# Performance work log

Measured on AMD Instinct MI355X. Metric: run time of the kernel, lower is better.

## Reference

```python
import jax, jax.numpy as jnp
import numpy as np

KH, KW = 3, 3
K = KH * KW
PAD, STRIDE, DIL = 1, 1, 1


def _conv(x, w, b):
    y = jax.lax.conv_general_dilated(
        x, w, (STRIDE, STRIDE), ((PAD, PAD), (PAD, PAD)),
        rhs_dilation=(DIL, DIL), dimension_numbers=('NCHW', 'OIHW', 'NCHW'))
    return y + b[None, :, None, None]


def _bilinear_gather(x, py, px):
    # x: [B,C,H,W]; py, px: float sample coords [B,K,Ho,Wo]. Zero outside bounds.
    B, C, H, W = x.shape
    y0 = jnp.floor(py)
    x0 = jnp.floor(px)
    wy1 = py - y0
    wx1 = px - x0
    wy0 = 1.0 - wy1
    wx0 = 1.0 - wx1
    xf = x.reshape(B, C, H * W)

    def g(yi, xi):
        valid = (yi >= 0) & (yi < H) & (xi >= 0) & (xi < W)
        yc = jnp.clip(yi, 0, H - 1).astype(jnp.int32)
        xc = jnp.clip(xi, 0, W - 1).astype(jnp.int32)
        idx = (yc * W + xc).reshape(B, -1)                      # [B, K*Ho*Wo]
        v = jax.vmap(lambda im, ix: im[:, ix])(xf, idx)         # [B, C, K*Ho*Wo]
        v = v.reshape(B, C, *yi.shape[1:])                      # [B,C,K,Ho,Wo]
        return v * valid[:, None].astype(x.dtype)

    return ((wy0 * wx0)[:, None] * g(y0, x0)
            + (wy0 * wx1)[:, None] * g(y0, x0 + 1)
            + (wy1 * wx0)[:, None] * g(y0 + 1, x0)
            + (wy1 * wx1)[:, None] * g(y0 + 1, x0 + 1))


def setup_inputs() -> dict:
    key = jax.random.key(0)
    k1, k2, k3 = jax.random.split(key, 3)
    B, C, H, W = 8, 256, 64, 64
    x = jax.random.normal(k1, (B, C, H, W), dtype=jnp.float32)
    # small init for offset/mask conv so predicted offsets stay modest (as in DCNv2 practice)
    w_om = jax.random.normal(k2, (3 * K, C, KH, KW), dtype=jnp.float32) * 0.01
    b_om = jnp.zeros((3 * K,), dtype=jnp.float32)
    w_dc = jax.random.normal(k3, (C, C, KH, KW), dtype=jnp.float32) * (1.0 / np.sqrt(C * K))
    b_dc = jnp.zeros((C,), dtype=jnp.float32)
    return {"x": x, "w_om": w_om, "b_om": b_om, "w_dc": w_dc, "b_dc": b_dc}


def reference(x, w_om, b_om, w_dc, b_dc):
    B, C, H, W = x.shape
    om = _conv(x, w_om, b_om)                      # [B, 3K, H, W]
    offset = om[:, :2 * K].reshape(B, K, 2, H, W)  # per-tap (dy, dx)
    mask = jax.nn.sigmoid(om[:, 2 * K:])           # [B, K, H, W]
    dy, dx = offset[:, :, 0], offset[:, :, 1]
    kh = jnp.repeat(jnp.arange(KH), KW)            # [K] kernel row index
    kw = jnp.tile(jnp.arange(KW), KH)              # [K] kernel col index
    ho = jnp.arange(H)
    wo = jnp.arange(W)
    py = ho[None, None, :, None] * STRIDE - PAD + kh[None, :, None, None] * DIL + dy
    px = wo[None, None, None, :] * STRIDE - PAD + kw[None, :, None, None] * DIL + dx
    sampled = _bilinear_gather(x, py, px)          # [B,C,K,H,W]
    sampled = sampled * mask[:, None]              # modulated (DCNv2)
    w = w_dc.reshape(w_dc.shape[0], C, K)
    out = jnp.einsum('bckhw,ock->bohw', sampled, w) + b_dc[None, :, None, None]
    return out
```

## Files before the change

### kernel.cpp

```cpp
#include <hip/hip_runtime.h>
#include <hip/hip_bf16.h>
#include <hip/hip_fp16.h>
#include <math.h>

#define BB   8
#define CIN  256
#define HH   64
#define WW   64
#define OMC  27
#define HW   (HH*WW)
#define KTOT (CIN*9)
#define NPIX 32
#define SPITCH 296
#define XP1    40
#define TPW    17

typedef short bf16x8 __attribute__((ext_vector_type(8)));
typedef float f32x4  __attribute__((ext_vector_type(4)));

__device__ __forceinline__ unsigned short f2bf(float f) {
    union { float f; unsigned int u; } v; v.f = f;
    unsigned int r = v.u + 0x7FFFu + ((v.u >> 16) & 1u);
    return (unsigned short)(r >> 16);
}
__device__ __forceinline__ float bflo(unsigned int a) {
    union { unsigned int u; float f; } c; c.u = a << 16; return c.f;
}
__device__ __forceinline__ float bfhi(unsigned int a) {
    union { unsigned int u; float f; } c; c.u = a & 0xFFFF0000u; return c.f;
}

__global__ __launch_bounds__(256) void wprep_kernel(
    const float* __restrict__ w_dc, unsigned short* __restrict__ wA)
{
    int e = blockIdx.x * 256 + threadIdx.x;
    int o = e / KTOT;
    int k = e - o * KTOT;
    int c   = k / 9;
    int tap = k - c * 9;
    int kp  = (c >> 5) * 288 + tap * 32 + (c & 31);
    wA[((size_t)(kp >> 3) * 256 + o) * 8 + (kp & 7)] = f2bf(w_dc[e]);
}

__global__ __launch_bounds__(256) void womprep_kernel(
    const float* __restrict__ w_om, unsigned short* __restrict__ wOmA)
{
    int e = blockIdx.x * 256 + threadIdx.x;
    int j  = e & 7;
    int t1 = e >> 3;
    int o  = t1 & 31;
    int t2 = t1 >> 5;
    int cb = t2 & 3;
    int t3 = t2 >> 2;
    int cc = t3 & 7;
    int tap = t3 >> 3;
    int c = cc * 32 + cb * 8 + j;
    float v = (o < OMC) ? w_om[(size_t)o * KTOT + c * 9 + tap] : 0.f;
    wOmA[e] = f2bf(v);
}

__global__ __launch_bounds__(512, 4) void deform_mfma_kernel(
    const float* __restrict__ x, const unsigned short* __restrict__ wOmA,
    const float* __restrict__ b_om,
    const unsigned short* __restrict__ wA, const float* __restrict__ b_dc,
    float* __restrict__ out)
{
    const int rawb = blockIdx.x;
    const int obid = ((rawb & 7) << 7) | (rawb >> 3);
    const int b    = obid >> 7;
    const int h    = (obid >> 1) & 63;
    const int w0   = (obid & 1) * NPIX;
    const int t    = threadIdx.x;
    const int wv   = t >> 6;
    const int lane = t & 63;
    const int lq   = lane >> 4;
    const int lm   = lane & 15;

    __shared__ __align__(16) unsigned short sS[NPIX * SPITCH];
    __shared__ __align__(16) unsigned short sR[8224];
    __shared__ __align__(16) int4 s_par[9 * NPIX];

    float* som  = reinterpret_cast<float*>(sS);
    unsigned short* bufA = sR;
    unsigned short* bufB = sR + 4080;

    const size_t xb_base = (size_t)b * CIN * HW;
    const float* gx_base = x + xb_base;

    int stg[7];
#pragma unroll
    for (int i = 0; i < 7; ++i) {
        int n = t + i * 512;
        if (n < 3200) {
            int slot = n / 200;
            int rc   = n - slot * 200;
            int r    = rc / 40;
            int c    = rc - r * 40;
            int gy   = min(max(h - 2 + r, 0), HH - 1);
            int gx   = min(max(w0 - 4 + c, 0), WW - 1);
            stg[i] = (rc * TPW + slot) | (slot << 12) | ((gy * WW + gx) << 16);
        } else stg[i] = -1;
    }

    {
        f32x4 accOm = (f32x4)(0.f);
        const int mfp = (wv >> 1) & 1;
        const int nfp = wv & 1;
        const int p   = nfp * 16 + lm;
        const bf16x8* wOmV = reinterpret_cast<const bf16x8*>(wOmA);

        auto stage1 = [&](int cc, unsigned short* dst) {
            const float* gch = gx_base + (size_t)cc * 32 * HW;
#pragma unroll
            for (int i = 0; i < 7; ++i) {
                int e = t + i * 512;
                if (e < 3264) {
                    int cl  = e / 102;
                    int rc  = e - cl * 102;
                    int row = rc / 34;
                    int col = rc - row * 34;
                    int gy  = h - 1 + row;
                    int gxx = w0 - 1 + col;
                    float v = 0.f;
                    if (gy >= 0 && gy < HH && (unsigned)gxx < WW)
                        v = gch[cl * HW + gy * WW + gxx];
                    dst[rc * XP1 + cl] = f2bf(v);
                }
            }
        };

        stage1(0, bufA);
        __syncthreads();
        for (int cc = 0; cc < 8; ++cc) {
            unsigned short* cur = (cc & 1) ? bufB : bufA;
            unsigned short* nxt = (cc & 1) ? bufA : bufB;
            if (cc < 7) stage1(cc + 1, nxt);
#pragma unroll
            for (int tap = 0; tap < 9; ++tap) {
                int kh = tap / 3, kw = tap % 3;
                bf16x8 bfr = *reinterpret_cast<const bf16x8*>(
                    &cur[(kh * 34 + p + kw) * XP1 + lq * 8]);
                bf16x8 af = wOmV[(((tap * 8 + cc) * 4 + lq) * 32) + mfp * 16 + lm];
                accOm = __builtin_amdgcn_mfma_f32_16x16x32_bf16(af, bfr, accOm, 0, 0, 0);
            }
            __syncthreads();
        }

        if (wv < 4) {
#pragma unroll
            for (int r = 0; r < 4; ++r) {
                int o = mfp * 16 + lq * 4 + r;
                if (o < OMC)
                    som[o * NPIX + p] = accOm[r] + b_om[o];
            }
        }
    }
    __syncthreads();

    float L0[7], L1[7];
    {
        const float* gch = gx_base;
#pragma unroll
        for (int i = 0; i < 7; ++i)
            if (stg[i] >= 0) {
                int sl = (stg[i] >> 12) & 0xF;
                int go = (stg[i] >> 16) & 0xFFF;
                L0[i] = gch[(size_t)(2 * sl) * HW + go];
                L1[i] = gch[(size_t)(2 * sl + 1) * HW + go];
            }
    }

    {
        unsigned int* tWw = reinterpret_cast<unsigned int*>(sR);
        for (int i = t; i < 712; i += 512) tWw[3400 + i] = 0u;
    }

    if (t < 9 * NPIX) {
        int tap = t >> 5;
        int pix = t & 31;
        float dy = som[(2 * tap) * NPIX + pix];
        float dx = som[(2 * tap + 1) * NPIX + pix];
        float mv = som[(18 + tap) * NPIX + pix];
        float m  = 1.f / (1.f + expf(-mv));
        float py = (float)(h - 1 + tap / 3) + dy;
        float px = (float)(w0 + pix - 1 + tap % 3) + dx;
        float y0f = floorf(py), x0f = floorf(px);
        float wy1 = py - y0f, wx1 = px - x0f;
        float wy0 = 1.f - wy1, wx0 = 1.f - wx1;
        int y0 = (int)y0f, x0 = (int)x0f;
        int y1 = y0 + 1, x1 = x0 + 1;
        bool yv0 = (y0 >= 0) && (y0 < HH);
        bool yv1 = (y1 >= 0) && (y1 < HH);
        bool xv0 = (x0 >= 0) && (x0 < WW);
        bool xv1 = (x1 >= 0) && (x1 < WW);
        int yc0 = min(max(y0, 0), HH - 1), yc1 = min(max(y1, 0), HH - 1);
        int xc0 = min(max(x0, 0), WW - 1), xc1 = min(max(x1, 0), WW - 1);
        float wwx = (yv0 && xv0) ? wy0 * wx0 * m : 0.f;
        float wwy = (yv0 && xv1) ? wy0 * wx1 * m : 0.f;
        float wwz = (yv1 && xv0) ? wy1 * wx0 * m : 0.f;
        float www = (yv1 && xv1) ? wy1 * wx1 * m : 0.f;
        if (xc1 == xc0) { wwx += wwy; wwy = 0.f; wwz += www; www = 0.f; }
        if (yc1 == yc0) { wwx += wwz; wwz = 0.f; wwy += www; www = 0.f; }
        bool inT = (yc0 >= h - 2) && (yc1 <= h + 2) &&
                   (xc0 >= w0 - 4) && (xc1 <= w0 + 35);
        int lb = (yc0 - (h - 2)) * 40 + (xc0 - (w0 - 4));
        int pk = (lb & 0xFF) | ((xc1 - xc0) << 8) | ((yc1 - yc0) << 9)
               | ((yc0 * WW + xc0) << 10);
        if (!inT) pk |= (int)0x80000000;
        __half2 wab = __floats2half2_rn(wwx, wwy);
        __half2 wcd = __floats2half2_rn(wwz, www);
        s_par[t] = make_int4(pk,
                             *reinterpret_cast<int*>(&wab),
                             *reinterpret_cast<int*>(&wcd), 0);
    }
    {
        unsigned int* tWw = reinterpret_cast<unsigned int*>(sR);
#pragma unroll
        for (int i = 0; i < 7; ++i)
            if (stg[i] >= 0)
                tWw[stg[i] & 0xFFF] =
                    f2bf(L0[i]) | ((unsigned int)f2bf(L1[i]) << 16);
    }
    __syncthreads();

    f32x4 acc[2][2];
#pragma unroll
    for (int i = 0; i < 2; ++i)
#pragma unroll
        for (int j = 0; j < 2; ++j)
            acc[i][j] = (f32x4)(0.f);

    const int pix  = t >> 4;
    const int slot = t & 15;
    const unsigned int* tW = reinterpret_cast<const unsigned int*>(sR);

    for (int ch = 0; ch < 8; ++ch) {
#pragma unroll 3
        for (int tap = 0; tap < 9; ++tap) {
            int idx = tap * NPIX + pix;
            int4 pv = s_par[idx];
            int pk  = pv.x;
            float2 wab = __half22float2(*reinterpret_cast<__half2*>(&pv.y));
            float2 wcd = __half22float2(*reinterpret_cast<__half2*>(&pv.z));
            float v0, v1;
            if (pk >= 0) {
                int base = (pk & 0xFF) * TPW + slot;
                unsigned int a00 = tW[base];
                unsigned int a01 = tW[base + TPW];
                unsigned int a10 = tW[base + 40 * TPW];
                unsigned int a11 = tW[base + 41 * TPW];
                v0 = wab.x * bflo(a00) + wab.y * bflo(a01)
                   + wcd.x * bflo(a10) + wcd.y * bflo(a11);
                v1 = wab.x * bfhi(a00) + wab.y * bfhi(a01)
                   + wcd.x * bfhi(a10) + wcd.y * bfhi(a11);
            } else {
                int off00 = (pk >> 10) & 0xFFF;
                int d01 = (pk >> 8) & 1;
                int d10 = ((pk >> 9) & 1) * WW;
                const float* xc = x + xb_base + (size_t)(ch * 32 + 2 * slot) * HW;
                v0 = wab.x * xc[off00]       + wab.y * xc[off00 + d01]
                   + wcd.x * xc[off00 + d10] + wcd.y * xc[off00 + d10 + d01];
                xc += HW;
                v1 = wab.x * xc[off00]       + wab.y * xc[off00 + d01]
                   + wcd.x * xc[off00 + d10] + wcd.y * xc[off00 + d10 + d01];
            }
            *reinterpret_cast<unsigned int*>(
                &sS[pix * SPITCH + tap * 32 + 2 * slot]) =
                f2bf(v0) | ((unsigned int)f2bf(v1) << 16);
        }
        __syncthreads();

        if (ch < 7) {
            const float* gch = gx_base + (size_t)(ch + 1) * 32 * HW;
#pragma unroll
            for (int i = 0; i < 7; ++i)
                if (stg[i] >= 0) {
                    int sl = (stg[i] >> 12) & 0xF;
                    int go = (stg[i] >> 16) & 0xFFF;
                    L0[i] = gch[(size_t)(2 * sl) * HW + go];
                    L1[i] = gch[(size_t)(2 * sl + 1) * HW + go];
                }
        }

        const int kb_base = ch * 36;
        const bf16x8* wAv = reinterpret_cast<const bf16x8*>(wA);
#pragma unroll 1
        for (int ks = 0; ks < 9; ++ks) {
            bf16x8 bfr[2];
#pragma unroll
            for (int nf = 0; nf < 2; ++nf)
                bfr[nf] = *reinterpret_cast<const bf16x8*>(
                    &sS[(nf * 16 + lm) * SPITCH + ks * 32 + lq * 8]);
#pragma unroll
            for (int mf = 0; mf < 2; ++mf) {
                int o  = wv * 32 + mf * 16 + lm;
                int kb = kb_base + ks * 4 + lq;
                bf16x8 af = wAv[(size_t)kb * 256 + o];
#pragma unroll
                for (int nf = 0; nf < 2; ++nf)
                    acc[mf][nf] = __builtin_amdgcn_mfma_f32_16x16x32_bf16(
                        af, bfr[nf], acc[mf][nf], 0, 0, 0);
            }
        }

        if (ch < 7) {
            unsigned int* tWw = reinterpret_cast<unsigned int*>(sR);
#pragma unroll
            for (int i = 0; i < 7; ++i)
                if (stg[i] >= 0)
                    tWw[stg[i] & 0xFFF] =
                        f2bf(L0[i]) | ((unsigned int)f2bf(L1[i]) << 16);
        }
        __syncthreads();
    }

#pragma unroll
    for (int mf = 0; mf < 2; ++mf) {
#pragma unroll
        for (int r = 0; r < 4; ++r) {
            int o = wv * 32 + mf * 16 + lq * 4 + r;
            float bo = b_dc[o];
#pragma unroll
            for (int nf = 0; nf < 2; ++nf) {
                int p = nf * 16 + lm;
                out[((size_t)(b * 256 + o)) * HW + h * WW + w0 + p] = acc[mf][nf][r] + bo;
            }
        }
    }
}

extern "C" void kernel_launch(void* const* d_in, const int* in_sizes, int n_in,
                              void* d_out, int out_size, void* d_ws, size_t ws_size,
                              hipStream_t stream) {
    const float* x    = (const float*)d_in[0];
    const float* w_om = (const float*)d_in[1];
    const float* b_om = (const float*)d_in[2];
    const float* w_dc = (const float*)d_in[3];
    const float* b_dc = (const float*)d_in[4];
    float* out = (float*)d_out;

    unsigned short* wA   = (unsigned short*)d_ws;
    unsigned short* wOmA = (unsigned short*)((char*)d_ws + 1179648);

    wprep_kernel<<<(256 * KTOT) / 256, 256, 0, stream>>>(w_dc, wA);
    womprep_kernel<<<73728 / 256, 256, 0, stream>>>(w_om, wOmA);
    deform_mfma_kernel<<<BB * HH * 2, 512, 0, stream>>>(x, wOmA, b_om, wA, b_dc, out);
}
```

Baseline: 152.3 us.

## Double-buffer staging and sample tiles to overlap gather with MFMA

Doubles both the bf16 input staging tile and the sampled-column tile in LDS. The bilinear gather for the next channel chunk, and the global load of the chunk after it, can then run in the same iteration as the MFMA GEMM on the current chunk. This removes one __syncthreads per chunk and is meant to hide gather and load latency behind matrix work. The cost is roughly double the LDS per block, which can lower the number of resident blocks per CU below the launch-bounds target of four.

```diff
diff --git a/kernel.cpp b/kernel.cpp
--- a/kernel.cpp
+++ b/kernel.cpp
@@ -12,8 +12,10 @@
 #define KTOT (CIN*9)
 #define NPIX 32
 #define SPITCH 296
+#define SSZ   (NPIX*SPITCH)
 #define XP1    40
 #define TPW    17
+#define TBUF   4096
 
 typedef short bf16x8 __attribute__((ext_vector_type(8)));
 typedef float f32x4  __attribute__((ext_vector_type(4)));
@@ -76,8 +78,8 @@
     const int lq   = lane >> 4;
     const int lm   = lane & 15;
 
-    __shared__ __align__(16) unsigned short sS[NPIX * SPITCH];
-    __shared__ __align__(16) unsigned short sR[8224];
+    __shared__ __align__(16) unsigned short sS[2 * SSZ];
+    __shared__ __align__(16) unsigned short sR[2 * TBUF * 2];
     __shared__ __align__(16) int4 s_par[9 * NPIX];
 
     float* som  = reinterpret_cast<float*>(sS);
@@ -157,9 +159,12 @@
     }
     __syncthreads();
 
+    unsigned int* tWw = reinterpret_cast<unsigned int*>(sR);
+    const unsigned int* tW = tWw;
+
     float L0[7], L1[7];
-    {
-        const float* gch = gx_base;
+    auto issueStage = [&](int ch) {
+        const float* gch = gx_base + (size_t)ch * 32 * HW;
 #pragma unroll
         for (int i = 0; i < 7; ++i)
             if (stg[i] >= 0) {
@@ -168,22 +173,73 @@
                 L0[i] = gch[(size_t)(2 * sl) * HW + go];
                 L1[i] = gch[(size_t)(2 * sl + 1) * HW + go];
             }
-    }
-
-    {
-        unsigned int* tWw = reinterpret_cast<unsigned int*>(sR);
-        for (int i = t; i < 712; i += 512) tWw[3400 + i] = 0u;
+    };
+    auto writeTile = [&](int buf) {
+        int off = buf << 12;
+#pragma unroll
+        for (int i = 0; i < 7; ++i)
+            if (stg[i] >= 0)
+                tWw[off + (stg[i] & 0xFFF)] =
+                    f2bf(L0[i]) | ((unsigned int)f2bf(L1[i]) << 16);
+    };
+
+    const int pix  = t >> 4;
+    const int slot = t & 15;
+
+    auto gather = [&](int ch) {
+        const int toff = (ch & 1) << 12;
+        unsigned short* sSc = sS + (ch & 1) * SSZ;
+#pragma unroll 3
+        for (int tap = 0; tap < 9; ++tap) {
+            int idx = tap * NPIX + pix;
+            int4 pv = s_par[idx];
+            int pk  = pv.x;
+            float2 wab = __half22float2(*reinterpret_cast<__half2*>(&pv.y));
+            float2 wcd = __half22float2(*reinterpret_cast<__half2*>(&pv.z));
+            float v0, v1;
+            if (pk >= 0) {
+                int base = toff + (pk & 0xFF) * TPW + slot;
+                unsigned int a00 = tW[base];
+                unsigned int a01 = tW[base + TPW];
+                unsigned int a10 = tW[base + 40 * TPW];
+                unsigned int a11 = tW[base + 41 * TPW];
+                v0 = wab.x * bflo(a00) + wab.y * bflo(a01)
+                   + wcd.x * bflo(a10) + wcd.y * bflo(a11);
+                v1 = wab.x * bfhi(a00) + wab.y * bfhi(a01)
+                   + wcd.x * bfhi(a10) + wcd.y * bfhi(a11);
+            } else {
+                int off00 = (pk >> 10) & 0xFFF;
+                int d01 = (pk >> 8) & 1;
+                int d10 = ((pk >> 9) & 1) * WW;
+                const float* xc = x + xb_base + (size_t)(ch * 32 + 2 * slot) * HW;
+                v0 = wab.x * xc[off00]       + wab.y * xc[off00 + d01]
+                   + wcd.x * xc[off00 + d10] + wcd.y * xc[off00 + d10 + d01];
+                xc += HW;
+                v1 = wab.x * xc[off00]       + wab.y * xc[off00 + d01]
+                   + wcd.x * xc[off00 + d10] + wcd.y * xc[off00 + d10 + d01];
+            }
+            *reinterpret_cast<unsigned int*>(
+                &sSc[pix * SPITCH + tap * 32 + 2 * slot]) =
+                f2bf(v0) | ((unsigned int)f2bf(v1) << 16);
+        }
+    };
+
+    issueStage(0);
+
+    for (int i = t; i < 1392; i += 512) {
+        int w = (i < 696) ? (3400 + i) : (4096 + 3400 + (i - 696));
+        tWw[w] = 0u;
     }
 
     if (t < 9 * NPIX) {
         int tap = t >> 5;
-        int pix = t & 31;
-        float dy = som[(2 * tap) * NPIX + pix];
-        float dx = som[(2 * tap + 1) * NPIX + pix];
-        float mv = som[(18 + tap) * NPIX + pix];
+        int pix2 = t & 31;
+        float dy = som[(2 * tap) * NPIX + pix2];
+        float dx = som[(2 * tap + 1) * NPIX + pix2];
+        float mv = som[(18 + tap) * NPIX + pix2];
         float m  = 1.f / (1.f + expf(-mv));
         float py = (float)(h - 1 + tap / 3) + dy;
-        float px = (float)(w0 + pix - 1 + tap % 3) + dx;
+        float px = (float)(w0 + pix2 - 1 + tap % 3) + dx;
         float y0f = floorf(py), x0f = floorf(px);
         float wy1 = py - y0f, wx1 = px - x0f;
         float wy0 = 1.f - wy1, wx0 = 1.f - wx1;
@@ -213,14 +269,12 @@
                              *reinterpret_cast<int*>(&wab),
                              *reinterpret_cast<int*>(&wcd), 0);
     }
-    {
-        unsigned int* tWw = reinterpret_cast<unsigned int*>(sR);
-#pragma unroll
-        for (int i = 0; i < 7; ++i)
-            if (stg[i] >= 0)
-                tWw[stg[i] & 0xFFF] =
-                    f2bf(L0[i]) | ((unsigned int)f2bf(L1[i]) << 16);
-    }
+    writeTile(0);
+    __syncthreads();
+
+    gather(0);
+    issueStage(1);
+    writeTile(1);
     __syncthreads();
 
     f32x4 acc[2][2];
@@ -230,67 +284,21 @@
         for (int j = 0; j < 2; ++j)
             acc[i][j] = (f32x4)(0.f);
 
-    const int pix  = t >> 4;
-    const int slot = t & 15;
-    const unsigned int* tW = reinterpret_cast<const unsigned int*>(sR);
+    const bf16x8* wAv = reinterpret_cast<const bf16x8*>(wA);
 
     for (int ch = 0; ch < 8; ++ch) {
-#pragma unroll 3
-        for (int tap = 0; tap < 9; ++tap) {
-            int idx = tap * NPIX + pix;
-            int4 pv = s_par[idx];
-            int pk  = pv.x;
-            float2 wab = __half22float2(*reinterpret_cast<__half2*>(&pv.y));
-            float2 wcd = __half22float2(*reinterpret_cast<__half2*>(&pv.z));
-            float v0, v1;
-            if (pk >= 0) {
-                int base = (pk & 0xFF) * TPW + slot;
-                unsigned int a00 = tW[base];
-                unsigned int a01 = tW[base + TPW];
-                unsigned int a10 = tW[base + 40 * TPW];
-                unsigned int a11 = tW[base + 41 * TPW];
-                v0 = wab.x * bflo(a00) + wab.y * bflo(a01)
-                   + wcd.x * bflo(a10) + wcd.y * bflo(a11);
-                v1 = wab.x * bfhi(a00) + wab.y * bfhi(a01)
-                   + wcd.x * bfhi(a10) + wcd.y * bfhi(a11);
-            } else {
-                int off00 = (pk >> 10) & 0xFFF;
-                int d01 = (pk >> 8) & 1;
-                int d10 = ((pk >> 9) & 1) * WW;
-                const float* xc = x + xb_base + (size_t)(ch * 32 + 2 * slot) * HW;
-                v0 = wab.x * xc[off00]       + wab.y * xc[off00 + d01]
-                   + wcd.x * xc[off00 + d10] + wcd.y * xc[off00 + d10 + d01];
-                xc += HW;
-                v1 = wab.x * xc[off00]       + wab.y * xc[off00 + d01]
-                   + wcd.x * xc[off00 + d10] + wcd.y * xc[off00 + d10 + d01];
-            }
-            *reinterpret_cast<unsigned int*>(
-                &sS[pix * SPITCH + tap * 32 + 2 * slot]) =
-                f2bf(v0) | ((unsigned int)f2bf(v1) << 16);
-        }
-        __syncthreads();
-
-        if (ch < 7) {
-            const float* gch = gx_base + (size_t)(ch + 1) * 32 * HW;
-#pragma unroll
-            for (int i = 0; i < 7; ++i)
-                if (stg[i] >= 0) {
-                    int sl = (stg[i] >> 12) & 0xF;
-                    int go = (stg[i] >> 16) & 0xFFF;
-                    L0[i] = gch[(size_t)(2 * sl) * HW + go];
-                    L1[i] = gch[(size_t)(2 * sl + 1) * HW + go];
-                }
-        }
-
+        if (ch < 6) issueStage(ch + 2);
+        if (ch < 7) gather(ch + 1);
+
+        const unsigned short* sSc = sS + (ch & 1) * SSZ;
         const int kb_base = ch * 36;
-        const bf16x8* wAv = reinterpret_cast<const bf16x8*>(wA);
 #pragma unroll 1
         for (int ks = 0; ks < 9; ++ks) {
             bf16x8 bfr[2];
 #pragma unroll
             for (int nf = 0; nf < 2; ++nf)
                 bfr[nf] = *reinterpret_cast<const bf16x8*>(
-                    &sS[(nf * 16 + lm) * SPITCH + ks * 32 + lq * 8]);
+                    &sSc[(nf * 16 + lm) * SPITCH + ks * 32 + lq * 8]);
 #pragma unroll
             for (int mf = 0; mf < 2; ++mf) {
                 int o  = wv * 32 + mf * 16 + lm;
@@ -303,14 +311,7 @@
             }
         }
 
-        if (ch < 7) {
-            unsigned int* tWw = reinterpret_cast<unsigned int*>(sR);
-#pragma unroll
-            for (int i = 0; i < 7; ++i)
-                if (stg[i] >= 0)
-                    tWw[stg[i] & 0xFFF] =
-                        f2bf(L0[i]) | ((unsigned int)f2bf(L1[i]) << 16);
-        }
+        if (ch < 6) writeTile(ch & 1);
         __syncthreads();
     }
 
```

Measured after the change: 156.0 us. 2.4% more time.

## Split offset/mask convolution into a separate full-row MFMA kernel

Applied to the files above, without the earlier changes.

Moves the offset/mask convolution out of the fused deformable kernel into its own kernel. Each block of the new kernel computes a full 64-pixel output row, using 2 M-fragments per wave, and writes the offsets and masks to a workspace buffer. The main kernel then reads the offsets from global memory instead of computing them, which removes the redundant halo staging and the 8-step synchronised prologue. The cost is an extra kernel launch plus a global round trip for the offset/mask tensor.

```diff
diff --git a/kernel.cpp b/kernel.cpp
--- a/kernel.cpp
+++ b/kernel.cpp
@@ -59,9 +59,83 @@
     wOmA[e] = f2bf(v);
 }
 
+__global__ __launch_bounds__(256, 4) void om_mfma_kernel(
+    const float* __restrict__ x, const unsigned short* __restrict__ wOmA,
+    const float* __restrict__ b_om, float* __restrict__ om)
+{
+    const int rawb = blockIdx.x;
+    const int obid = ((rawb & 7) << 6) | (rawb >> 3);
+    const int b    = obid >> 6;
+    const int h    = obid & 63;
+    const int t    = threadIdx.x;
+    const int wv   = t >> 6;
+    const int lane = t & 63;
+    const int lq   = lane >> 4;
+    const int lm   = lane & 15;
+    const int p    = wv * 16 + lm;
+
+    __shared__ __align__(16) unsigned short sX[2 * 3 * 66 * XP1];
+
+    unsigned short* bufA = sX;
+    unsigned short* bufB = sX + 3 * 66 * XP1;
+
+    const size_t xb_base = (size_t)b * CIN * HW;
+    const float* gx_base = x + xb_base;
+    const bf16x8* wOmV = reinterpret_cast<const bf16x8*>(wOmA);
+
+    f32x4 accOm[2];
+    accOm[0] = (f32x4)(0.f);
+    accOm[1] = (f32x4)(0.f);
+
+    auto stage1 = [&](int cc, unsigned short* dst) {
+        const float* gch = gx_base + (size_t)cc * 32 * HW;
+        for (int e = t; e < 3 * 66 * 32; e += 256) {
+            int cl  = e / 198;
+            int rc  = e - cl * 198;
+            int row = rc / 66;
+            int col = rc - row * 66;
+            int gy  = h - 1 + row;
+            int gxx = col - 1;
+            float v = 0.f;
+            if (gy >= 0 && gy < HH && (unsigned)gxx < WW)
+                v = gch[cl * HW + gy * WW + gxx];
+            dst[rc * XP1 + cl] = f2bf(v);
+        }
+    };
+
+    stage1(0, bufA);
+    __syncthreads();
+    for (int cc = 0; cc < 8; ++cc) {
+        unsigned short* cur = (cc & 1) ? bufB : bufA;
+        unsigned short* nxt = (cc & 1) ? bufA : bufB;
+        if (cc < 7) stage1(cc + 1, nxt);
+#pragma unroll
+        for (int tap = 0; tap < 9; ++tap) {
+            int kh = tap / 3, kw = tap % 3;
+            bf16x8 bfr = *reinterpret_cast<const bf16x8*>(
+                &cur[(kh * 66 + p + kw) * XP1 + lq * 8]);
+#pragma unroll
+            for (int mf = 0; mf < 2; ++mf) {
+                bf16x8 af = wOmV[(((tap * 8 + cc) * 4 + lq) * 32) + mf * 16 + lm];
+                accOm[mf] = __builtin_amdgcn_mfma_f32_16x16x32_bf16(
+                    af, bfr, accOm[mf], 0, 0, 0);
+            }
+        }
+        __syncthreads();
+    }
+
+#pragma unroll
+    for (int mf = 0; mf < 2; ++mf)
+#pragma unroll
+        for (int r = 0; r < 4; ++r) {
+            int o = mf * 16 + lq * 4 + r;
+            if (o < OMC)
+                om[((size_t)(b * OMC + o) * HH + h) * WW + p] = accOm[r >= 0 ? mf : mf][r] + b_om[o];
+        }
+}
+
 __global__ __launch_bounds__(512, 4) void deform_mfma_kernel(
-    const float* __restrict__ x, const unsigned short* __restrict__ wOmA,
-    const float* __restrict__ b_om,
+    const float* __restrict__ x, const float* __restrict__ om,
     const unsigned short* __restrict__ wA, const float* __restrict__ b_dc,
     float* __restrict__ out)
 {
@@ -80,10 +154,6 @@
     __shared__ __align__(16) unsigned short sR[8224];
     __shared__ __align__(16) int4 s_par[9 * NPIX];
 
-    float* som  = reinterpret_cast<float*>(sS);
-    unsigned short* bufA = sR;
-    unsigned short* bufB = sR + 4080;
-
     const size_t xb_base = (size_t)b * CIN * HW;
     const float* gx_base = x + xb_base;
 
@@ -102,60 +172,8 @@
         } else stg[i] = -1;
     }
 
-    {
-        f32x4 accOm = (f32x4)(0.f);
-        const int mfp = (wv >> 1) & 1;
-        const int nfp = wv & 1;
-        const int p   = nfp * 16 + lm;
-        const bf16x8* wOmV = reinterpret_cast<const bf16x8*>(wOmA);
-
-        auto stage1 = [&](int cc, unsigned short* dst) {
-            const float* gch = gx_base + (size_t)cc * 32 * HW;
-#pragma unroll
-            for (int i = 0; i < 7; ++i) {
-                int e = t + i * 512;
-                if (e < 3264) {
-                    int cl  = e / 102;
-                    int rc  = e - cl * 102;
-                    int row = rc / 34;
-                    int col = rc - row * 34;
-                    int gy  = h - 1 + row;
-                    int gxx = w0 - 1 + col;
-                    float v = 0.f;
-                    if (gy >= 0 && gy < HH && (unsigned)gxx < WW)
-                        v = gch[cl * HW + gy * WW + gxx];
-                    dst[rc * XP1 + cl] = f2bf(v);
-                }
-            }
-        };
-
-        stage1(0, bufA);
-        __syncthreads();
-        for (int cc = 0; cc < 8; ++cc) {
-            unsigned short* cur = (cc & 1) ? bufB : bufA;
-            unsigned short* nxt = (cc & 1) ? bufA : bufB;
-            if (cc < 7) stage1(cc + 1, nxt);
-#pragma unroll
-            for (int tap = 0; tap < 9; ++tap) {
-                int kh = tap / 3, kw = tap % 3;
-                bf16x8 bfr = *reinterpret_cast<const bf16x8*>(
-                    &cur[(kh * 34 + p + kw) * XP1 + lq * 8]);
-                bf16x8 af = wOmV[(((tap * 8 + cc) * 4 + lq) * 32) + mfp * 16 + lm];
-                accOm = __builtin_amdgcn_mfma_f32_16x16x32_bf16(af, bfr, accOm, 0, 0, 0);
-            }
-            __syncthreads();
-        }
-
-        if (wv < 4) {
-#pragma unroll
-            for (int r = 0; r < 4; ++r) {
-                int o = mfp * 16 + lq * 4 + r;
-                if (o < OMC)
-                    som[o * NPIX + p] = accOm[r] + b_om[o];
-            }
-        }
-    }
-    __syncthreads();
+    unsigned int* tWw = reinterpret_cast<unsigned int*>(sR);
+    const unsigned int* tW = tWw;
 
     float L0[7], L1[7];
     {
@@ -170,17 +188,15 @@
             }
     }
 
-    {
-        unsigned int* tWw = reinterpret_cast<unsigned int*>(sR);
-        for (int i = t; i < 712; i += 512) tWw[3400 + i] = 0u;
-    }
+    for (int i = t; i < 712; i += 512) tWw[3400 + i] = 0u;
 
     if (t < 9 * NPIX) {
         int tap = t >> 5;
         int pix = t & 31;
-        float dy = som[(2 * tap) * NPIX + pix];
-        float dx = som[(2 * tap + 1) * NPIX + pix];
-        float mv = som[(18 + tap) * NPIX + pix];
+        const float* omb = om + ((size_t)b * OMC * HH + h) * WW + w0 + pix;
+        float dy = omb[(size_t)(2 * tap) * HW];
+        float dx = omb[(size_t)(2 * tap + 1) * HW];
+        float mv = omb[(size_t)(18 + tap) * HW];
         float m  = 1.f / (1.f + expf(-mv));
         float py = (float)(h - 1 + tap / 3) + dy;
         float px = (float)(w0 + pix - 1 + tap % 3) + dx;
@@ -214,7 +230,6 @@
                              *reinterpret_cast<int*>(&wcd), 0);
     }
     {
-        unsigned int* tWw = reinterpret_cast<unsigned int*>(sR);
 #pragma unroll
         for (int i = 0; i < 7; ++i)
             if (stg[i] >= 0)
@@ -232,7 +247,6 @@
 
     const int pix  = t >> 4;
     const int slot = t & 15;
-    const unsigned int* tW = reinterpret_cast<const unsigned int*>(sR);
 
     for (int ch = 0; ch < 8; ++ch) {
 #pragma unroll 3
@@ -304,7 +318,6 @@
         }
 
         if (ch < 7) {
-            unsigned int* tWw = reinterpret_cast<unsigned int*>(sR);
 #pragma unroll
             for (int i = 0; i < 7; ++i)
                 if (stg[i] >= 0)
@@ -341,8 +354,10 @@
 
     unsigned short* wA   = (unsigned short*)d_ws;
     unsigned short* wOmA = (unsigned short*)((char*)d_ws + 1179648);
+    float*          om   = (float*)((char*)d_ws + 1327104);
 
     wprep_kernel<<<(256 * KTOT) / 256, 256, 0, stream>>>(w_dc, wA);
     womprep_kernel<<<73728 / 256, 256, 0, stream>>>(w_om, wOmA);
-    deform_mfma_kernel<<<BB * HH * 2, 512, 0, stream>>>(x, wOmA, b_om, wA, b_dc, out);
-}
+    om_mfma_kernel<<<BB * HH, 256, 0, stream>>>(x, wOmA, b_om, om);
+    deform_mfma_kernel<<<BB * HH * 2, 512, 0, stream>>>(x, om, wA, b_dc, out);
+}
```

New measurement: 190.4 us. 25.0% more time.

## Split offset/mask conv into separate split-K kernel with atomic accumulation

Applied to the files above, without the earlier changes.

Moves the offset/mask 3x3 convolution out of the fused deformable kernel into its own MFMA kernel. That kernel uses twice as many blocks, each covering half the input channels, and combines the halves with atomicAdd into a bias-initialised global buffer. The deformable kernel then reads offsets and masks from global memory instead of computing them in shared memory. The aim is more parallelism for the offset conv and a shorter main kernel, at the cost of two extra launches, a global round-trip for the offsets, and atomics.

```diff
diff --git a/kernel.cpp b/kernel.cpp
--- a/kernel.cpp
+++ b/kernel.cpp
@@ -59,9 +59,94 @@
     wOmA[e] = f2bf(v);
 }
 
+__global__ __launch_bounds__(256) void om_init_kernel(
+    const float* __restrict__ b_om, float* __restrict__ om)
+{
+    int e = blockIdx.x * 256 + threadIdx.x;
+    om[e] = b_om[(e / HW) % OMC];
+}
+
+__global__ __launch_bounds__(512, 4) void om_mfma_kernel(
+    const float* __restrict__ x, const unsigned short* __restrict__ wOmA,
+    float* __restrict__ om)
+{
+    const int rawb = blockIdx.x;
+    const int obid = ((rawb & 7) << 8) | (rawb >> 3);
+    const int b    = obid >> 8;
+    const int h    = (obid >> 2) & 63;
+    const int w0   = ((obid >> 1) & 1) * 32;
+    const int ksp  = obid & 1;
+    const int t    = threadIdx.x;
+    const int wv   = t >> 6;
+    const int lane = t & 63;
+    const int lq   = lane >> 4;
+    const int lm   = lane & 15;
+    const int mfp  = (wv >> 1) & 1;
+    const int nfp  = wv & 1;
+    const int p    = nfp * 16 + lm;
+
+    __shared__ __align__(16) unsigned short sX[2 * 102 * XP1];
+
+    unsigned short* bufA = sX;
+    unsigned short* bufB = sX + 102 * XP1;
+
+    const size_t xb_base = (size_t)b * CIN * HW;
+    const float* gx_base = x + xb_base;
+    const bf16x8* wOmV = reinterpret_cast<const bf16x8*>(wOmA);
+
+    f32x4 accOm = (f32x4)(0.f);
+
+    auto stage1 = [&](int cc, unsigned short* dst) {
+        const float* gch = gx_base + (size_t)cc * 32 * HW;
+#pragma unroll
+        for (int i = 0; i < 7; ++i) {
+            int e = t + i * 512;
+            if (e < 102 * 32) {
+                int cl  = e / 102;
+                int rc  = e - cl * 102;
+                int row = rc / 34;
+                int col = rc - row * 34;
+                int gy  = h - 1 + row;
+                int gxx = w0 - 1 + col;
+                float v = 0.f;
+                if (gy >= 0 && gy < HH && (unsigned)gxx < WW)
+                    v = gch[cl * HW + gy * WW + gxx];
+                dst[rc * XP1 + cl] = f2bf(v);
+            }
+        }
+    };
+
+    stage1(ksp * 4, bufA);
+    __syncthreads();
+    for (int q = 0; q < 4; ++q) {
+        const int ch = ksp * 4 + q;
+        unsigned short* cur = (q & 1) ? bufB : bufA;
+        unsigned short* nxt = (q & 1) ? bufA : bufB;
+        if (q < 3) stage1(ch + 1, nxt);
+#pragma unroll
+        for (int tap = 0; tap < 9; ++tap) {
+            int th = tap / 3, tw = tap % 3;
+            bf16x8 bfr = *reinterpret_cast<const bf16x8*>(
+                &cur[(th * 34 + p + tw) * XP1 + lq * 8]);
+            bf16x8 af = wOmV[(((tap * 8 + ch) * 4 + lq) * 32) + mfp * 16 + lm];
+            accOm = __builtin_amdgcn_mfma_f32_16x16x32_bf16(af, bfr, accOm, 0, 0, 0);
+        }
+        __syncthreads();
+    }
+
+    if (wv < 4) {
+#pragma unroll
+        for (int r = 0; r < 4; ++r) {
+            int o = mfp * 16 + lq * 4 + r;
+            if (o < OMC)
+                atomicAdd(&om[((size_t)(b * OMC + o) * HH + h) * WW + w0 + p],
+                          accOm[r]);
+        }
+    }
+}
+
 __global__ __launch_bounds__(512, 4) void deform_mfma_kernel(
-    const float* __restrict__ x, const unsigned short* __restrict__ wOmA,
-    const float* __restrict__ b_om,
+    const float* __restrict__ x, const float* __restrict__ om,
     const unsigned short* __restrict__ wA, const float* __restrict__ b_dc,
     float* __restrict__ out)
 {
@@ -79,10 +164,6 @@
     __shared__ __align__(16) unsigned short sS[NPIX * SPITCH];
     __shared__ __align__(16) unsigned short sR[8224];
     __shared__ __align__(16) int4 s_par[9 * NPIX];
-
-    float* som  = reinterpret_cast<float*>(sS);
-    unsigned short* bufA = sR;
-    unsigned short* bufB = sR + 4080;
 
     const size_t xb_base = (size_t)b * CIN * HW;
     const float* gx_base = x + xb_base;
@@ -102,60 +183,8 @@
         } else stg[i] = -1;
     }
 
-    {
-        f32x4 accOm = (f32x4)(0.f);
-        const int mfp = (wv >> 1) & 1;
-        const int nfp = wv & 1;
-        const int p   = nfp * 16 + lm;
-        const bf16x8* wOmV = reinterpret_cast<const bf16x8*>(wOmA);
-
-        auto stage1 = [&](int cc, unsigned short* dst) {
-            const float* gch = gx_base + (size_t)cc * 32 * HW;
-#pragma unroll
-            for (int i = 0; i < 7; ++i) {
-                int e = t + i * 512;
-                if (e < 3264) {
-                    int cl  = e / 102;
-                    int rc  = e - cl * 102;
-                    int row = rc / 34;
-                    int col = rc - row * 34;
-                    int gy  = h - 1 + row;
-                    int gxx = w0 - 1 + col;
-                    float v = 0.f;
-                    if (gy >= 0 && gy < HH && (unsigned)gxx < WW)
-                        v = gch[cl * HW + gy * WW + gxx];
-                    dst[rc * XP1 + cl] = f2bf(v);
-                }
-            }
-        };
-
-        stage1(0, bufA);
-        __syncthreads();
-        for (int cc = 0; cc < 8; ++cc) {
-            unsigned short* cur = (cc & 1) ? bufB : bufA;
-            unsigned short* nxt = (cc & 1) ? bufA : bufB;
-            if (cc < 7) stage1(cc + 1, nxt);
-#pragma unroll
-            for (int tap = 0; tap < 9; ++tap) {
-                int kh = tap / 3, kw = tap % 3;
-                bf16x8 bfr = *reinterpret_cast<const bf16x8*>(
-                    &cur[(kh * 34 + p + kw) * XP1 + lq * 8]);
-                bf16x8 af = wOmV[(((tap * 8 + cc) * 4 + lq) * 32) + mfp * 16 + lm];
-                accOm = __builtin_amdgcn_mfma_f32_16x16x32_bf16(af, bfr, accOm, 0, 0, 0);
-            }
-            __syncthreads();
-        }
-
-        if (wv < 4) {
-#pragma unroll
-            for (int r = 0; r < 4; ++r) {
-                int o = mfp * 16 + lq * 4 + r;
-                if (o < OMC)
-                    som[o * NPIX + p] = accOm[r] + b_om[o];
-            }
-        }
-    }
-    __syncthreads();
+    unsigned int* tWw = reinterpret_cast<unsigned int*>(sR);
+    const unsigned int* tW = tWw;
 
     float L0[7], L1[7];
     {
@@ -170,17 +199,15 @@
             }
     }
 
-    {
-        unsigned int* tWw = reinterpret_cast<unsigned int*>(sR);
-        for (int i = t; i < 712; i += 512) tWw[3400 + i] = 0u;
-    }
+    for (int i = t; i < 712; i += 512) tWw[3400 + i] = 0u;
 
     if (t < 9 * NPIX) {
         int tap = t >> 5;
         int pix = t & 31;
-        float dy = som[(2 * tap) * NPIX + pix];
-        float dx = som[(2 * tap + 1) * NPIX + pix];
-        float mv = som[(18 + tap) * NPIX + pix];
+        const float* omb = om + ((size_t)b * OMC * HH + h) * WW + w0 + pix;
+        float dy = omb[(size_t)(2 * tap) * HW];
+        float dx = omb[(size_t)(2 * tap + 1) * HW];
+        float mv = omb[(size_t)(18 + tap) * HW];
         float m  = 1.f / (1.f + expf(-mv));
         float py = (float)(h - 1 + tap / 3) + dy;
         float px = (float)(w0 + pix - 1 + tap % 3) + dx;
@@ -214,7 +241,6 @@
                              *reinterpret_cast<int*>(&wcd), 0);
     }
     {
-        unsigned int* tWw = reinterpret_cast<unsigned int*>(sR);
 #pragma unroll
         for (int i = 0; i < 7; ++i)
             if (stg[i] >= 0)
@@ -232,7 +258,6 @@
 
     const int pix  = t >> 4;
     const int slot = t & 15;
-    const unsigned int* tW = reinterpret_cast<const unsigned int*>(sR);
 
     for (int ch = 0; ch < 8; ++ch) {
 #pragma unroll 3
@@ -304,7 +329,6 @@
         }
 
         if (ch < 7) {
-            unsigned int* tWw = reinterpret_cast<unsigned int*>(sR);
 #pragma unroll
             for (int i = 0; i < 7; ++i)
                 if (stg[i] >= 0)
@@ -341,8 +365,11 @@
 
     unsigned short* wA   = (unsigned short*)d_ws;
     unsigned short* wOmA = (unsigned short*)((char*)d_ws + 1179648);
+    float*          om   = (float*)((char*)d_ws + 1327104);
 
     wprep_kernel<<<(256 * KTOT) / 256, 256, 0, stream>>>(w_dc, wA);
     womprep_kernel<<<73728 / 256, 256, 0, stream>>>(w_om, wOmA);
-    deform_mfma_kernel<<<BB * HH * 2, 512, 0, stream>>>(x, wOmA, b_om, wA, b_dc, out);
-}
+    om_init_kernel<<<(BB * OMC * HW) / 256, 256, 0, stream>>>(b_om, om);
+    om_mfma_kernel<<<BB * HH * 4, 512, 0, stream>>>(x, wOmA, om);
+    deform_mfma_kernel<<<BB * HH * 2, 512, 0, stream>>>(x, om, wA, b_dc, out);
+}
```

New measurement: 165.3 us. 1.09x slower.
